# Optimization experiments

Hardware: AMD Instinct MI355X
Metric: run time of the kernel (lower is better)

## Reference

```python
import jax, jax.numpy as jnp
import numpy as np

N_NODES = 50000
N_EDGES = 400000
IN_DIM = 512
HID = 512
HID2 = HID // 2
OUT_DIM = 2
NUM_GRAPHS = 500


def setup_inputs() -> dict:
    key = jax.random.key(0)
    ks = jax.random.split(key, 12)
    x = jax.random.normal(ks[0], (N_NODES, IN_DIM), dtype=jnp.float32)
    edge_index = jax.random.randint(ks[1], (2, N_EDGES), 0, N_NODES, dtype=jnp.int64)
    batch = jnp.sort(jax.random.randint(ks[2], (N_NODES,), 0, NUM_GRAPHS, dtype=jnp.int64))
    def lin(k, fan_out, fan_in):
        bound = 1.0 / np.sqrt(fan_in)
        return jax.random.uniform(k, (fan_out, fan_in), jnp.float32, -bound, bound)
    # SAGEConv layer 1: lin_l (on aggregated neighbors, with bias) + lin_r (root)
    W1l = lin(ks[3], HID, IN_DIM)
    b1 = jax.random.uniform(ks[4], (HID,), jnp.float32, -1/np.sqrt(IN_DIM), 1/np.sqrt(IN_DIM))
    W1r = lin(ks[5], HID, IN_DIM)
    # SAGEConv layer 2
    W2l = lin(ks[6], HID2, HID)
    b2 = jax.random.uniform(ks[7], (HID2,), jnp.float32, -1/np.sqrt(HID), 1/np.sqrt(HID))
    W2r = lin(ks[8], HID2, HID)
    # final fc
    Wfc = lin(ks[9], OUT_DIM, HID2)
    bfc = jax.random.uniform(ks[10], (OUT_DIM,), jnp.float32, -1/np.sqrt(HID2), 1/np.sqrt(HID2))
    return {"x": x, "edge_index": edge_index, "batch": batch,
            "W1l": W1l, "b1": b1, "W1r": W1r,
            "W2l": W2l, "b2": b2, "W2r": W2r,
            "Wfc": Wfc, "bfc": bfc}


def _sage_conv(h, src, dst, Wl, bl, Wr):
    # mean-aggregate source features into target nodes, then linear + root term
    n = h.shape[0]
    agg = jax.ops.segment_sum(h[src], dst, num_segments=n)          # [N, d_in]
    deg = jax.ops.segment_sum(jnp.ones(src.shape, h.dtype), dst, num_segments=n)
    agg = agg / jnp.maximum(deg, 1.0)[:, None]
    return agg @ Wl.T + bl + h @ Wr.T


def reference(x, edge_index, batch, W1l, b1, W1r, W2l, b2, W2r, Wfc, bfc):
    src, dst = edge_index[0], edge_index[1]
    h = jax.nn.relu(_sage_conv(x, src, dst, W1l, b1, W1r))
    h = jax.nn.relu(_sage_conv(h, src, dst, W2l, b2, W2r))
    # global mean pool over graph ids
    pooled = jax.ops.segment_sum(h, batch, num_segments=NUM_GRAPHS)  # [G, HID2]
    counts = jax.ops.segment_sum(jnp.ones(batch.shape, h.dtype), batch, num_segments=NUM_GRAPHS)
    pooled = pooled / jnp.maximum(counts, 1.0)[:, None]
    logits = pooled @ Wfc.T + bfc
    return jax.nn.log_softmax(logits, axis=1)
```

## Files before the change

### kernel.cpp

```cpp
#include <hip/hip_runtime.h>
#include <cstdint>

#define N_NODES 50000
#define N_PAD 50048
#define N_EDGES 400000
#define IN_DIM 512
#define HID 512
#define HID2 256
#define NUM_GRAPHS 500
#define SCAN_BLOCKS 196

typedef unsigned short u16;
typedef short s8v __attribute__((ext_vector_type(8)));
typedef float f4v __attribute__((ext_vector_type(4)));
typedef u16 u16x8 __attribute__((ext_vector_type(8)));

__device__ __forceinline__ u16 f2bf(float f) {
  union { float f; uint32_t u; } c;
  c.f = f;
  const uint32_t u = c.u;
  return (u16)((u + 0x7fffu + ((u >> 16) & 1u)) >> 16);
}
__device__ __forceinline__ float bf2f(u16 v) {
  union { uint32_t u; float f; } c;
  c.u = ((uint32_t)v) << 16;
  return c.f;
}

__device__ __forceinline__ void gload16(const void* g, void* l) {
  __builtin_amdgcn_global_load_lds(
      (const __attribute__((address_space(1))) void*)(uintptr_t)g,
      (__attribute__((address_space(3))) void*)(uint32_t)(uintptr_t)l, 16, 0, 0);
}

__device__ __forceinline__ int xcd_swizzle(int orig, int nwg) {
  const int q = nwg >> 3, rr = nwg & 7;
  const int xcd = orig & 7, idx = orig >> 3;
  return (xcd < rr ? xcd * (q + 1) : rr * (q + 1) + (xcd - rr) * q) + idx;
}

__global__ __launch_bounds__(256) void cvt_f32_bf16(const float* __restrict__ in,
                                                    u16* __restrict__ out, int n8) {
  const int i = blockIdx.x * 256 + threadIdx.x;
  if (i >= n8) return;
  const float4 a = ((const float4*)in)[2 * i];
  const float4 b = ((const float4*)in)[2 * i + 1];
  u16x8 o;
  o[0] = f2bf(a.x); o[1] = f2bf(a.y); o[2] = f2bf(a.z); o[3] = f2bf(a.w);
  o[4] = f2bf(b.x); o[5] = f2bf(b.y); o[6] = f2bf(b.z); o[7] = f2bf(b.w);
  ((u16x8*)out)[i] = o;
}

__global__ __launch_bounds__(256) void cvt_weights(const float* __restrict__ W1l,
                                                   const float* __restrict__ W1r,
                                                   const float* __restrict__ W2l,
                                                   const float* __restrict__ W2r,
                                                   u16* __restrict__ Wc1,
                                                   u16* __restrict__ Wc2) {
  const int i = blockIdx.x * 256 + threadIdx.x;
  const float* src;
  u16* dstp;
  int l;
  if (i < 32768)      { src = W1l; dstp = Wc1;          l = i; }
  else if (i < 65536) { src = W1r; dstp = Wc1 + 262144; l = i - 32768; }
  else if (i < 81920) { src = W2l; dstp = Wc2;          l = i - 65536; }
  else                { src = W2r; dstp = Wc2 + 131072; l = i - 81920; }
  const float4 a = ((const float4*)src)[2 * l];
  const float4 b = ((const float4*)src)[2 * l + 1];
  u16x8 o;
  o[0] = f2bf(a.x); o[1] = f2bf(a.y); o[2] = f2bf(a.z); o[3] = f2bf(a.w);
  o[4] = f2bf(b.x); o[5] = f2bf(b.y); o[6] = f2bf(b.z); o[7] = f2bf(b.w);
  ((u16x8*)dstp)[l] = o;
}

__global__ __launch_bounds__(256) void gemm_mfma(const u16* __restrict__ A,
                                                 const u16* __restrict__ B,
                                                 u16* __restrict__ CT,
                                                 u16* __restrict__ CR,
                                                 int K, int nxLog2, int nxHalf,
                                                 int nwg) {
  __shared__ __align__(16) u16 As[128 * 32];
  __shared__ __align__(16) u16 Bs[128 * 32];
  const int id = xcd_swizzle(blockIdx.x, nwg);
  const int bx = id & ((1 << nxLog2) - 1);
  const int by = id >> nxLog2;
  const int tid = threadIdx.x;
  const int lane = tid & 63;
  const int wave = tid >> 6;
  const int wr = (wave >> 1) * 64;
  const int wc = (wave & 1) * 64;
  const int fr = lane & 15;
  const int fq = lane >> 4;
  const size_t bm = (size_t)by * 128;
  const size_t bn = (size_t)bx * 128;

  const int r0 = tid >> 2;
  const int c0 = (tid & 3) * 8;
  const u16* gA = A + (bm + r0) * K + c0;
  const u16* gB = B + (bn + r0) * K + c0;
  u16* lA = As + r0 * 32 + c0;
  u16* lB = Bs + r0 * 32 + c0;
  const size_t rstep = (size_t)64 * K;

  f4v acc[4][4];
#pragma unroll
  for (int m = 0; m < 4; ++m)
#pragma unroll
    for (int n = 0; n < 4; ++n)
      acc[m][n] = f4v{0.f, 0.f, 0.f, 0.f};

  for (int k0 = 0; k0 < K; k0 += 32) {
    __syncthreads();
    gload16(gA + k0, lA);
    gload16(gA + rstep + k0, lA + 64 * 32);
    gload16(gB + k0, lB);
    gload16(gB + rstep + k0, lB + 64 * 32);
    __syncthreads();
    s8v af[4], bf_[4];
#pragma unroll
    for (int m = 0; m < 4; ++m)
      af[m] = *(const s8v*)(As + (wr + m * 16 + fr) * 32 + fq * 8);
#pragma unroll
    for (int n = 0; n < 4; ++n)
      bf_[n] = *(const s8v*)(Bs + (wc + n * 16 + fr) * 32 + fq * 8);
#pragma unroll
    for (int m = 0; m < 4; ++m)
#pragma unroll
      for (int n = 0; n < 4; ++n)
        acc[m][n] = __builtin_amdgcn_mfma_f32_16x16x32_bf16(af[m], bf_[n],
                                                            acc[m][n], 0, 0, 0);
  }

  u16* Cb = (bx < nxHalf) ? CT : CR;
  const int ldc = nxHalf * 128;
  const size_t cn0 = (size_t)(bx - (bx >= nxHalf ? nxHalf : 0)) * 128 + wc;
#pragma unroll
  for (int m = 0; m < 4; ++m) {
    const size_t row0 = bm + wr + m * 16 + fq * 4;
#pragma unroll
    for (int n = 0; n < 4; ++n) {
      const size_t col = cn0 + n * 16 + fr;
#pragma unroll
      for (int i = 0; i < 4; ++i)
        Cb[(row0 + i) * ldc + col] = f2bf(acc[m][n][i]);
    }
  }
}

__global__ void deg_hist(const int* __restrict__ dst, int* __restrict__ degi, int nE) {
  const int e = blockIdx.x * 256 + threadIdx.x;
  if (e < nE) atomicAdd(&degi[dst[e]], 1);
}

__device__ __forceinline__ int block_scan_excl(int v, int* total_out) {
  const int lane = threadIdx.x & 63;
  const int wid = threadIdx.x >> 6;
  int s = v;
#pragma unroll
  for (int off = 1; off < 64; off <<= 1) {
    const int t = __shfl_up(s, off);
    if (lane >= off) s += t;
  }
  __shared__ int wsum[4];
  if (lane == 63) wsum[wid] = s;
  __syncthreads();
  int base = 0;
#pragma unroll
  for (int w = 0; w < 4; ++w)
    if (w < wid) base += wsum[w];
  *total_out = wsum[0] + wsum[1] + wsum[2] + wsum[3];
  return base + s - v;
}

__global__ __launch_bounds__(256) void scan_blocks(const int* __restrict__ degi,
                                                   int* __restrict__ offs,
                                                   int* __restrict__ bsum, int n) {
  const int gid = blockIdx.x * 256 + threadIdx.x;
  const int v = (gid < n) ? degi[gid] : 0;
  int total;
  const int excl = block_scan_excl(v, &total);
  if (gid < n) offs[gid] = excl;
  if (threadIdx.x == 0) bsum[blockIdx.x] = total;
}

__global__ __launch_bounds__(256) void scan_bsums(int* __restrict__ bsum, int nb) {
  const int v = (threadIdx.x < nb) ? bsum[threadIdx.x] : 0;
  int total;
  const int excl = block_scan_excl(v, &total);
  if (threadIdx.x < nb) bsum[threadIdx.x] = excl;
}

__global__ __launch_bounds__(256) void add_base(int* __restrict__ offs,
                                                const int* __restrict__ bsum,
                                                int n, int nE) {
  const int gid = blockIdx.x * 256 + threadIdx.x;
  if (gid < n) offs[gid] += bsum[blockIdx.x];
  if (gid == 0) offs[n] = nE;
}

__global__ void fill_csr(const int* __restrict__ src, const int* __restrict__ dst,
                         const int* __restrict__ offs, int* __restrict__ cursor,
                         int* __restrict__ sorted_src, int nE) {
  const int e = blockIdx.x * 256 + threadIdx.x;
  if (e < nE) {
    const int d = dst[e];
    const int pos = offs[d] + atomicAdd(&cursor[d], 1);
    sorted_src[pos] = src[e];
  }
}

template <int D, int OUTF32>
__global__ __launch_bounds__(256) void gather_combine(
    const u16* __restrict__ t, const u16* __restrict__ r,
    const float* __restrict__ bias, const int* __restrict__ offs,
    const int* __restrict__ ssrc, void* __restrict__ hout) {
  constexpr int LPN = D / 8;
  const int node = (int)((blockIdx.x * 256u + threadIdx.x) / LPN);
  if (node >= N_NODES) return;
  const int o = (int)(threadIdx.x % LPN) * 8;
  const int beg = offs[node], end = offs[node + 1];
  float a[8] = {0.f, 0.f, 0.f, 0.f, 0.f, 0.f, 0.f, 0.f};
  int e = beg;
  for (; e + 3 < end; e += 4) {
    const int s0 = ssrc[e], s1 = ssrc[e + 1], s2 = ssrc[e + 2], s3 = ssrc[e + 3];
    const u16x8 v0 = *(const u16x8*)(t + (size_t)s0 * D + o);
    const u16x8 v1 = *(const u16x8*)(t + (size_t)s1 * D + o);
    const u16x8 v2 = *(const u16x8*)(t + (size_t)s2 * D + o);
    const u16x8 v3 = *(const u16x8*)(t + (size_t)s3 * D + o);
#pragma unroll
    for (int j = 0; j < 8; ++j)
      a[j] += (bf2f(v0[j]) + bf2f(v1[j])) + (bf2f(v2[j]) + bf2f(v3[j]));
  }
  for (; e < end; ++e) {
    const u16x8 v0 = *(const u16x8*)(t + (size_t)ssrc[e] * D + o);
#pragma unroll
    for (int j = 0; j < 8; ++j) a[j] += bf2f(v0[j]);
  }
  const float invd = 1.0f / fmaxf((float)(end - beg), 1.0f);
  const u16x8 rv = *(const u16x8*)(r + (size_t)node * D + o);
  float hv[8];
#pragma unroll
  for (int j = 0; j < 8; ++j)
    hv[j] = fmaxf(fmaf(a[j], invd, bias[o + j] + bf2f(rv[j])), 0.f);
  if (OUTF32) {
    float* hp = (float*)hout + (size_t)node * D + o;
    *(float4*)hp = make_float4(hv[0], hv[1], hv[2], hv[3]);
    *(float4*)(hp + 4) = make_float4(hv[4], hv[5], hv[6], hv[7]);
  } else {
    u16x8 ov;
#pragma unroll
    for (int j = 0; j < 8; ++j) ov[j] = f2bf(hv[j]);
    *(u16x8*)((u16*)hout + (size_t)node * D + o) = ov;
  }
}

__global__ __launch_bounds__(256) void pool_final(const float* __restrict__ h,
                                                  const int* __restrict__ batch,
                                                  const float* __restrict__ Wfc,
                                                  const float* __restrict__ bfc,
                                                  float* __restrict__ out, int nNodes) {
  const int g = blockIdx.x;
  __shared__ int sbeg, send;
  if (threadIdx.x == 0) {
    int lo = 0, hi = nNodes;
    while (lo < hi) { const int mid = (lo + hi) >> 1; if (batch[mid] < g) lo = mid + 1; else hi = mid; }
    sbeg = lo;
    hi = nNodes;
    while (lo < hi) { const int mid = (lo + hi) >> 1; if (batch[mid] < g + 1) lo = mid + 1; else hi = mid; }
    send = lo;
  }
  __syncthreads();
  const int t = threadIdx.x;
  float s = 0.f;
  for (int row = sbeg; row < send; ++row) s += h[(size_t)row * HID2 + t];
  const float cnt = fmaxf((float)(send - sbeg), 1.0f);
  const float p = s / cnt;
  float d0 = p * Wfc[t];
  float d1 = p * Wfc[HID2 + t];
#pragma unroll
  for (int off = 32; off > 0; off >>= 1) {
    d0 += __shfl_down(d0, off);
    d1 += __shfl_down(d1, off);
  }
  __shared__ float r0[4], r1[4];
  const int wid = t >> 6, lane = t & 63;
  if (lane == 0) { r0[wid] = d0; r1[wid] = d1; }
  __syncthreads();
  if (t == 0) {
    const float l0 = r0[0] + r0[1] + r0[2] + r0[3] + bfc[0];
    const float l1 = r1[0] + r1[1] + r1[2] + r1[3] + bfc[1];
    const float m = fmaxf(l0, l1);
    const float lse = m + logf(expf(l0 - m) + expf(l1 - m));
    out[g * 2 + 0] = l0 - lse;
    out[g * 2 + 1] = l1 - lse;
  }
}

extern "C" void kernel_launch(void* const* d_in, const int* in_sizes, int n_in,
                              void* d_out, int out_size, void* d_ws, size_t ws_size,
                              hipStream_t stream) {
  (void)in_sizes; (void)n_in; (void)out_size; (void)ws_size;
  const float* x   = (const float*)d_in[0];
  const int* eidx  = (const int*)d_in[1];
  const int* batch = (const int*)d_in[2];
  const float* W1l = (const float*)d_in[3];
  const float* b1  = (const float*)d_in[4];
  const float* W1r = (const float*)d_in[5];
  const float* W2l = (const float*)d_in[6];
  const float* b2  = (const float*)d_in[7];
  const float* W2r = (const float*)d_in[8];
  const float* Wfc = (const float*)d_in[9];
  const float* bfc = (const float*)d_in[10];
  float* out = (float*)d_out;
  const int* src = eidx;
  const int* dst = eidx + N_EDGES;

  char* ws = (char*)d_ws;
  size_t off = 0;
  auto alloc = [&](size_t bytes) {
    char* p = ws + off;
    off += (bytes + 255) & ~(size_t)255;
    return p;
  };
  u16* bufT = (u16*)alloc((size_t)N_PAD * 512 * 2);
  u16* bufR = (u16*)alloc((size_t)N_PAD * 512 * 2);
  u16* bufX = (u16*)alloc((size_t)N_PAD * 512 * 2);
  u16* h1   = (u16*)alloc((size_t)N_PAD * 512 * 2);
  u16* Wc1  = (u16*)alloc((size_t)1024 * 512 * 2);
  u16* Wc2  = (u16*)alloc((size_t)512 * 512 * 2);
  int* degi       = (int*)alloc((size_t)N_NODES * 4);
  int* offs       = (int*)alloc((size_t)(N_NODES + 1) * 4);
  int* cursor     = (int*)alloc((size_t)N_NODES * 4);
  int* sorted_src = (int*)alloc((size_t)N_EDGES * 4);
  int* bsum       = (int*)alloc((size_t)SCAN_BLOCKS * 4);
  float* h2 = (float*)bufX;

  hipMemsetAsync(degi, 0, (size_t)N_NODES * 4, stream);
  hipMemsetAsync(cursor, 0, (size_t)N_NODES * 4, stream);
  deg_hist<<<(N_EDGES + 255) / 256, 256, 0, stream>>>(dst, degi, N_EDGES);
  scan_blocks<<<SCAN_BLOCKS, 256, 0, stream>>>(degi, offs, bsum, N_NODES);
  scan_bsums<<<1, 256, 0, stream>>>(bsum, SCAN_BLOCKS);
  add_base<<<SCAN_BLOCKS, 256, 0, stream>>>(offs, bsum, N_NODES, N_EDGES);
  fill_csr<<<(N_EDGES + 255) / 256, 256, 0, stream>>>(src, dst, offs, cursor,
                                                      sorted_src, N_EDGES);

  cvt_f32_bf16<<<(N_NODES * (IN_DIM / 8) + 255) / 256, 256, 0, stream>>>(
      x, bufX, N_NODES * (IN_DIM / 8));
  cvt_weights<<<384, 256, 0, stream>>>(W1l, W1r, W2l, W2r, Wc1, Wc2);

  {
    const int nwg = (N_PAD / 128) * 8;
    gemm_mfma<<<nwg, 256, 0, stream>>>(bufX, Wc1, bufT, bufR, IN_DIM, 3, 4, nwg);
  }
  gather_combine<HID, 0><<<(N_NODES + 3) / 4, 256, 0, stream>>>(
      bufT, bufR, b1, offs, sorted_src, h1);

  {
    const int nwg = (N_PAD / 128) * 4;
    gemm_mfma<<<nwg, 256, 0, stream>>>(h1, Wc2, bufT, bufR, HID, 2, 2, nwg);
  }
  gather_combine<HID2, 1><<<(N_NODES + 7) / 8, 256, 0, stream>>>(
      bufT, bufR, b2, offs, sorted_src, h2);

  pool_final<<<NUM_GRAPHS, 256, 0, stream>>>(h2, batch, Wfc, bfc, out, N_NODES);
}
```

Measured before the change: 359.1 us.

## Double-buffer GEMM LDS tiles with async prefetch and vectorized transposed stores

The MFMA GEMM now keeps two LDS buffers and prefetches the k-tile two steps ahead, using explicit vmcnt waits and raw barriers so global loads overlap the MFMA work. The MFMA operands are swapped so each lane holds four consecutive output columns, which lets the epilogue write them as one 8-byte vector store instead of four scalar stores. K and the grid shape become template parameters so the loop is fully specialised. The two memsets are merged into one by placing degi and cursor next to each other. LDS use doubles, which may reduce occupancy, and the hand-written waitcnt sequencing risks a data race if the count of outstanding loads is wrong.

```diff
diff --git a/kernel.cpp b/kernel.cpp
--- a/kernel.cpp
+++ b/kernel.cpp
@@ -14,6 +14,7 @@
 typedef short s8v __attribute__((ext_vector_type(8)));
 typedef float f4v __attribute__((ext_vector_type(4)));
 typedef u16 u16x8 __attribute__((ext_vector_type(8)));
+typedef u16 u16x4 __attribute__((ext_vector_type(4)));
 
 __device__ __forceinline__ u16 f2bf(float f) {
   union { float f; uint32_t u; } c;
@@ -73,17 +74,17 @@
   ((u16x8*)dstp)[l] = o;
 }
 
+template <int K, int NXL2, int NXH>
 __global__ __launch_bounds__(256) void gemm_mfma(const u16* __restrict__ A,
                                                  const u16* __restrict__ B,
                                                  u16* __restrict__ CT,
                                                  u16* __restrict__ CR,
-                                                 int K, int nxLog2, int nxHalf,
                                                  int nwg) {
-  __shared__ __align__(16) u16 As[128 * 32];
-  __shared__ __align__(16) u16 Bs[128 * 32];
+  __shared__ __align__(16) u16 As[2][128 * 32];
+  __shared__ __align__(16) u16 Bs[2][128 * 32];
   const int id = xcd_swizzle(blockIdx.x, nwg);
-  const int bx = id & ((1 << nxLog2) - 1);
-  const int by = id >> nxLog2;
+  const int bx = id & ((1 << NXL2) - 1);
+  const int by = id >> NXL2;
   const int tid = threadIdx.x;
   const int lane = tid & 63;
   const int wave = tid >> 6;
@@ -98,9 +99,17 @@
   const int c0 = (tid & 3) * 8;
   const u16* gA = A + (bm + r0) * K + c0;
   const u16* gB = B + (bn + r0) * K + c0;
-  u16* lA = As + r0 * 32 + c0;
-  u16* lB = Bs + r0 * 32 + c0;
   const size_t rstep = (size_t)64 * K;
+  const int lofs = r0 * 32 + c0;
+  constexpr int nt = K >> 5;
+
+  auto stage = [&](int b, int kt) {
+    const int k0 = kt << 5;
+    gload16(gA + k0, &As[b][lofs]);
+    gload16(gA + rstep + k0, &As[b][lofs + 64 * 32]);
+    gload16(gB + k0, &Bs[b][lofs]);
+    gload16(gB + rstep + k0, &Bs[b][lofs + 64 * 32]);
+  };
 
   f4v acc[4][4];
 #pragma unroll
@@ -109,40 +118,51 @@
     for (int n = 0; n < 4; ++n)
       acc[m][n] = f4v{0.f, 0.f, 0.f, 0.f};
 
-  for (int k0 = 0; k0 < K; k0 += 32) {
-    __syncthreads();
-    gload16(gA + k0, lA);
-    gload16(gA + rstep + k0, lA + 64 * 32);
-    gload16(gB + k0, lB);
-    gload16(gB + rstep + k0, lB + 64 * 32);
-    __syncthreads();
+  stage(0, 0);
+  stage(1, 1);
+  asm volatile("s_waitcnt vmcnt(4)" ::: "memory");
+  __builtin_amdgcn_s_barrier();
+
+  for (int t = 0; t < nt; ++t) {
+    const u16* curA = As[t & 1];
+    const u16* curB = Bs[t & 1];
     s8v af[4], bf_[4];
 #pragma unroll
     for (int m = 0; m < 4; ++m)
-      af[m] = *(const s8v*)(As + (wr + m * 16 + fr) * 32 + fq * 8);
+      af[m] = *(const s8v*)(curA + (wr + m * 16 + fr) * 32 + fq * 8);
 #pragma unroll
     for (int n = 0; n < 4; ++n)
-      bf_[n] = *(const s8v*)(Bs + (wc + n * 16 + fr) * 32 + fq * 8);
+      bf_[n] = *(const s8v*)(curB + (wc + n * 16 + fr) * 32 + fq * 8);
 #pragma unroll
     for (int m = 0; m < 4; ++m)
 #pragma unroll
       for (int n = 0; n < 4; ++n)
-        acc[m][n] = __builtin_amdgcn_mfma_f32_16x16x32_bf16(af[m], bf_[n],
+        acc[m][n] = __builtin_amdgcn_mfma_f32_16x16x32_bf16(bf_[n], af[m],
                                                             acc[m][n], 0, 0, 0);
-  }
-
-  u16* Cb = (bx < nxHalf) ? CT : CR;
-  const int ldc = nxHalf * 128;
-  const size_t cn0 = (size_t)(bx - (bx >= nxHalf ? nxHalf : 0)) * 128 + wc;
+    if (t == nt - 1) break;
+    __builtin_amdgcn_s_barrier();
+    if (t + 2 < nt) {
+      stage(t & 1, t + 2);
+      asm volatile("s_waitcnt vmcnt(4)" ::: "memory");
+    } else {
+      asm volatile("s_waitcnt vmcnt(0)" ::: "memory");
+    }
+    __builtin_amdgcn_s_barrier();
+  }
+
+  u16* Cb = (bx < NXH) ? CT : CR;
+  constexpr int ldc = NXH * 128;
+  const size_t cn0 = (size_t)(bx - (bx >= NXH ? NXH : 0)) * 128 + wc;
 #pragma unroll
   for (int m = 0; m < 4; ++m) {
-    const size_t row0 = bm + wr + m * 16 + fq * 4;
+    const size_t row = bm + wr + m * 16 + fr;
 #pragma unroll
     for (int n = 0; n < 4; ++n) {
-      const size_t col = cn0 + n * 16 + fr;
-#pragma unroll
-      for (int i = 0; i < 4; ++i)
-        Cb[(row0 + i) * ldc + col] = f2bf(acc[m][n][i]);
+      const size_t col = cn0 + n * 16 + fq * 4;
+      u16x4 p;
+#pragma unroll
+      for (int i = 0; i < 4; ++i) p[i] = f2bf(acc[m][n][i]);
+      *(u16x4*)(Cb + row * ldc + col) = p;
     }
   }
 }
@@ -328,15 +348,14 @@
   u16* h1   = (u16*)alloc((size_t)N_PAD * 512 * 2);
   u16* Wc1  = (u16*)alloc((size_t)1024 * 512 * 2);
   u16* Wc2  = (u16*)alloc((size_t)512 * 512 * 2);
-  int* degi       = (int*)alloc((size_t)N_NODES * 4);
+  int* degi   = (int*)alloc((size_t)N_NODES * 4);
+  int* cursor = (int*)alloc((size_t)N_NODES * 4);
   int* offs       = (int*)alloc((size_t)(N_NODES + 1) * 4);
-  int* cursor     = (int*)alloc((size_t)N_NODES * 4);
   int* sorted_src = (int*)alloc((size_t)N_EDGES * 4);
   int* bsum       = (int*)alloc((size_t)SCAN_BLOCKS * 4);
   float* h2 = (float*)bufX;
 
-  hipMemsetAsync(degi, 0, (size_t)N_NODES * 4, stream);
-  hipMemsetAsync(cursor, 0, (size_t)N_NODES * 4, stream);
+  hipMemsetAsync(degi, 0, 200192 + (size_t)N_NODES * 4, stream);
   deg_hist<<<(N_EDGES + 255) / 256, 256, 0, stream>>>(dst, degi, N_EDGES);
   scan_blocks<<<SCAN_BLOCKS, 256, 0, stream>>>(degi, offs, bsum, N_NODES);
   scan_bsums<<<1, 256, 0, stream>>>(bsum, SCAN_BLOCKS);
@@ -350,14 +369,14 @@
 
   {
     const int nwg = (N_PAD / 128) * 8;
-    gemm_mfma<<<nwg, 256, 0, stream>>>(bufX, Wc1, bufT, bufR, IN_DIM, 3, 4, nwg);
+    gemm_mfma<IN_DIM, 3, 4><<<nwg, 256, 0, stream>>>(bufX, Wc1, bufT, bufR, nwg);
   }
   gather_combine<HID, 0><<<(N_NODES + 3) / 4, 256, 0, stream>>>(
       bufT, bufR, b1, offs, sorted_src, h1);
 
   {
     const int nwg = (N_PAD / 128) * 4;
-    gemm_mfma<<<nwg, 256, 0, stream>>>(h1, Wc2, bufT, bufR, HID, 2, 2, nwg);
+    gemm_mfma<HID, 2, 2><<<nwg, 256, 0, stream>>>(h1, Wc2, bufT, bufR, nwg);
   }
   gather_combine<HID2, 1><<<(N_NODES + 7) / 8, 256, 0, stream>>>(
       bufT, bufR, b2, offs, sorted_src, h2);
```

New measurement: 350.6 us. 2.4% less time.
